# Kernel optimization log

Hardware: AMD Instinct MI355X
Metric: run time of the kernel (lower is better)

The kernel has to match this reference:

```python
import jax, jax.numpy as jnp
import numpy as np

B, S, D, H = 2, 2048, 512, 8


def setup_inputs() -> dict:
    key = jax.random.key(0)
    ks = jax.random.split(key, 9)
    scale = 1.0 / np.sqrt(D)
    x = jax.random.normal(ks[0], (B, S, D), dtype=jnp.float32)
    # Per-head full-width projections, stacked over heads: [H, D, D]
    Wq = jax.random.normal(ks[1], (H, D, D), dtype=jnp.float32) * scale
    Wk = jax.random.normal(ks[2], (H, D, D), dtype=jnp.float32) * scale
    Wv = jax.random.normal(ks[3], (H, D, D), dtype=jnp.float32) * scale
    bq = jax.random.normal(ks[4], (H, D), dtype=jnp.float32) * 0.01
    bk = jax.random.normal(ks[5], (H, D), dtype=jnp.float32) * 0.01
    bv = jax.random.normal(ks[6], (H, D), dtype=jnp.float32) * 0.01
    Wo = jax.random.normal(ks[7], (H * D, D), dtype=jnp.float32) * (1.0 / np.sqrt(H * D))
    bo = jax.random.normal(ks[8], (D,), dtype=jnp.float32) * 0.01
    return {"x": x, "Wq": Wq, "bq": bq, "Wk": Wk, "bk": bk, "Wv": Wv, "bv": bv, "Wo": Wo, "bo": bo}


def reference(x, Wq, bq, Wk, bk, Wv, bv, Wo, bo):
    # Batched per-head projections: [B,S,D] x [H,D,E] -> [B,H,S,E]
    q = jnp.einsum('bsd,hde->bhse', x, Wq) + bq[None, :, None, :]
    k = jnp.einsum('bsd,hde->bhse', x, Wk) + bk[None, :, None, :]
    v = jnp.einsum('bsd,hde->bhse', x, Wv) + bv[None, :, None, :]
    # NOTE: original module has NO 1/sqrt(d) scaling
    scores = jnp.einsum('bhse,bhte->bhst', q, k)  # [B,H,S,S]
    attn = jax.nn.softmax(scores, axis=-1)
    out = jnp.einsum('bhst,bhte->bhse', attn, v)  # [B,H,S,D]
    # Concat heads along feature dim: [B,S,H*D]
    cat = out.transpose(0, 2, 1, 3).reshape(B, S, H * D)
    return cat @ Wo + bo
```

## Files before the change

### kernel.cpp

```cpp
#include <hip/hip_runtime.h>

typedef _Float16 f16;
typedef _Float16 f16x8 __attribute__((ext_vector_type(8)));
typedef float f32x4 __attribute__((ext_vector_type(4)));

#define B_ 2
#define S_ 2048
#define D_ 512
#define H_ 8

__device__ inline void async_ld16(const void* g, void* l) {
  __builtin_amdgcn_global_load_lds((__attribute__((address_space(1))) void*)(g),
                                   (__attribute__((address_space(3))) void*)(l),
                                   16, 0, 0);
}

__global__ __launch_bounds__(256) void cvt_f16(const float* __restrict__ src,
                                               f16* __restrict__ dst, long n) {
  long i = (long)blockIdx.x * 256 + threadIdx.x;
  if (i >= n) return;
  dst[i] = (f16)src[i];
}

__global__ __launch_bounds__(256) void transpose_f32(const float* __restrict__ src,
                                                     f16* __restrict__ dst, int R, int C) {
  __shared__ float t[32][33];
  size_t zoff = (size_t)blockIdx.z * R * C;
  const float* s = src + zoff;
  int tx = threadIdx.x;
  int ty = threadIdx.y;
  int c0 = blockIdx.x * 32, r0 = blockIdx.y * 32;
#pragma unroll
  for (int i = 0; i < 4; ++i)
    t[ty + i * 8][tx] = s[(size_t)(r0 + ty + i * 8) * C + c0 + tx];
  __syncthreads();
#pragma unroll
  for (int i = 0; i < 4; ++i)
    dst[zoff + (size_t)(c0 + ty + i * 8) * R + r0 + tx] = (f16)t[tx][ty + i * 8];
}

__global__ __launch_bounds__(256) void reduce_out(const float* __restrict__ part,
                                                  const float* __restrict__ bo,
                                                  float* __restrict__ out, long n, int nslab) {
  long i = (long)blockIdx.x * 256 + threadIdx.x;
  if (i >= n) return;
  float v = bo[i & (D_ - 1)];
  for (int s = 0; s < nslab; ++s) v += part[(long)s * n + i];
  out[i] = v;
}

struct GemmArgs {
  const f16 *A, *Bm;
  void* C;
  const float* bias;
  float* Mloc;
  int K, lda, ldb, ldc;
  int zbase, NG, PBG;
  long sAp, sAb, sAg, sAz;
  long sBp, sBb, sBg, sBz;
  long sCp, sCb, sCg, sCz;
  long sbp, sbb, sbg, sbz;
  long sMlz;
};

template <typename OutT, int BIAS, bool PEXP>
__global__ __launch_bounds__(256) void gemm_nt(GemmArgs p) {
  int zloc = blockIdx.z;
  int zi = p.zbase + zloc;
  int pp = zi / p.PBG; int rz = zi - pp * p.PBG;
  int bb = rz / p.NG;  int g = rz - bb * p.NG;
  const f16* A  = p.A + (pp * p.sAp + bb * p.sAb + g * p.sAg + (long)zloc * p.sAz);
  const f16* Bm = p.Bm + (pp * p.sBp + bb * p.sBb + g * p.sBg + (long)zloc * p.sBz);
  OutT* C = (OutT*)p.C + (pp * p.sCp + bb * p.sCb + g * p.sCg + (long)zloc * p.sCz);
  const float* bias = nullptr;
  if (BIAS) bias = p.bias + (pp * p.sbp + bb * p.sbb + g * p.sbg + (long)zloc * p.sbz);

  __shared__ f16 lA[4096];
  __shared__ f16 lB[4096];
  __shared__ float lMx[PEXP ? 256 : 1];
  __shared__ f16 lR[PEXP ? 32 * 136 : 1];

  int tid = threadIdx.x;
  int lane = tid & 63;
  int w = tid >> 6;
  int wm = (w >> 1) << 6;
  int wn = (w & 1) << 6;
  long bm = (long)blockIdx.y * 128;
  long bn = (long)blockIdx.x * 128;

  f32x4 acc[4][4] = {};
  int qd = lane >> 4;
  int fr = lane & 15;

  int q0 = tid, q1 = tid + 256;
  int r0s = q0 >> 2, c0s = (q0 & 3) ^ ((r0s >> 1) & 3);
  int r1s = q1 >> 2, c1s = (q1 & 3) ^ ((r1s >> 1) & 3);

  for (int k0 = 0; k0 < p.K; k0 += 32) {
    long oa0 = (bm + r0s) * (long)p.lda + (k0 + c0s * 8);
    long oa1 = (bm + r1s) * (long)p.lda + (k0 + c1s * 8);
    long ob0 = (bn + r0s) * (long)p.ldb + (k0 + c0s * 8);
    long ob1 = (bn + r1s) * (long)p.ldb + (k0 + c1s * 8);
    __syncthreads();
    async_ld16(A + oa0,  lA + (size_t)q0 * 8);
    async_ld16(A + oa1,  lA + (size_t)q1 * 8);
    async_ld16(Bm + ob0, lB + (size_t)q0 * 8);
    async_ld16(Bm + ob1, lB + (size_t)q1 * 8);
    __syncthreads();

    f16x8 ah[4], bh[4];
#pragma unroll
    for (int i = 0; i < 4; ++i) {
      int m = wm + i * 16 + fr;
      ah[i] = *(const f16x8*)(lA + ((size_t)m * 4 + (qd ^ ((m >> 1) & 3))) * 8);
      int n = wn + i * 16 + fr;
      bh[i] = *(const f16x8*)(lB + ((size_t)n * 4 + (qd ^ ((n >> 1) & 3))) * 8);
    }
#pragma unroll
    for (int i = 0; i < 4; ++i)
#pragma unroll
      for (int j = 0; j < 4; ++j)
        acc[i][j] = __builtin_amdgcn_mfma_f32_16x16x32_f16(ah[i], bh[j], acc[i][j], 0, 0, 0);
  }

  int rr0 = qd * 4;
  if (PEXP) {
#pragma unroll
    for (int i = 0; i < 4; ++i) {
#pragma unroll
      for (int r = 0; r < 4; ++r) {
        float v = fmaxf(fmaxf(acc[i][0][r], acc[i][1][r]),
                        fmaxf(acc[i][2][r], acc[i][3][r]));
        v = fmaxf(v, __shfl_xor(v, 1, 64));
        v = fmaxf(v, __shfl_xor(v, 2, 64));
        v = fmaxf(v, __shfl_xor(v, 4, 64));
        v = fmaxf(v, __shfl_xor(v, 8, 64));
        if (fr == 0) lMx[(w & 1) * 128 + wm + i * 16 + rr0 + r] = v;
      }
    }
    __syncthreads();
    if (tid < 128) {
      float ml = fmaxf(lMx[tid], lMx[128 + tid]);
      p.Mloc[(long)zloc * p.sMlz + (long)blockIdx.x * S_ + bm + tid] = ml;
    }
    int rowBase = (w >> 1) << 4;
#pragma unroll
    for (int i = 0; i < 4; ++i) {
      __syncthreads();
#pragma unroll
      for (int r = 0; r < 4; ++r) {
        int rl = wm + i * 16 + rr0 + r;
        float ml = fmaxf(lMx[rl], lMx[128 + rl]);
        int rowLoc = rowBase + rr0 + r;
#pragma unroll
        for (int j = 0; j < 4; ++j) {
          int col = wn + j * 16 + fr;
          lR[rowLoc * 136 + col] = (f16)__expf(acc[i][j][r] - ml);
        }
      }
      __syncthreads();
      int rowLoc = tid >> 3;
      int colLoc = (tid & 7) * 16;
      long grow = bm + ((rowLoc & 15) + i * 16) + ((long)(rowLoc >> 4) << 6);
      f16x8 v0 = *(const f16x8*)(lR + rowLoc * 136 + colLoc);
      f16x8 v1 = *(const f16x8*)(lR + rowLoc * 136 + colLoc + 8);
      f16* dst = (f16*)C + grow * (long)p.ldc + bn + colLoc;
      *(f16x8*)(dst) = v0;
      *(f16x8*)(dst + 8) = v1;
    }
  } else {
#pragma unroll
    for (int i = 0; i < 4; ++i) {
#pragma unroll
      for (int j = 0; j < 4; ++j) {
#pragma unroll
        for (int r = 0; r < 4; ++r) {
          long row = bm + wm + i * 16 + rr0 + r;
          long col = bn + wn + j * 16 + fr;
          float v = acc[i][j][r];
          if (BIAS == 1) v += bias[col];
          if (BIAS == 2) v += bias[row];
          C[row * (long)p.ldc + col] = (OutT)v;
        }
      }
    }
  }
}

struct QkvArgs {
  const f16 *xh, *wqk, *wv;
  f16 *qk, *vT;
  const float *bqk, *bv;
};
__global__ __launch_bounds__(256) void qkv_proj(QkvArgs p) {
  const long SD = (long)S_ * D_, DD = (long)D_ * D_, DS = (long)D_ * S_;
  int zi = blockIdx.z;
  int pp = zi >> 4;
  int r = zi & 15;
  int b = r >> 3, h = r & 7;
  int bid = blockIdx.x;
  const f16 *A, *Bm;
  f16* C;
  const float* bias;
  long bm, bn;
  int ldc;
  bool biasRow;
  if (pp < 2) {
    A = p.xh + (long)b * SD;
    Bm = p.wqk + ((long)pp * 8 + h) * DD;
    C = p.qk + (long)zi * SD;
    bias = p.bqk + ((long)pp * 8 + h) * D_;
    bm = (long)(bid >> 2) * 128; bn = (long)(bid & 3) * 128;
    ldc = D_; biasRow = false;
  } else {
    A = p.wv + (long)h * DD;
    Bm = p.xh + (long)b * SD;
    C = p.vT + (long)(b * 8 + h) * DS;
    bias = p.bv + (long)h * D_;
    bm = (long)(bid >> 4) * 128; bn = (long)(bid & 15) * 128;
    ldc = S_; biasRow = true;
  }

  __shared__ f16 lA[4096];
  __shared__ f16 lB[4096];

  int tid = threadIdx.x;
  int lane = tid & 63;
  int w = tid >> 6;
  int wm = (w >> 1) << 6;
  int wn = (w & 1) << 6;

  f32x4 acc[4][4] = {};
  int qd = lane >> 4;
  int fr = lane & 15;

  int q0 = tid, q1 = tid + 256;
  int r0s = q0 >> 2, c0s = (q0 & 3) ^ ((r0s >> 1) & 3);
  int r1s = q1 >> 2, c1s = (q1 & 3) ^ ((r1s >> 1) & 3);

  for (int k0 = 0; k0 < D_; k0 += 32) {
    long oa0 = (bm + r0s) * (long)D_ + (k0 + c0s * 8);
    long oa1 = (bm + r1s) * (long)D_ + (k0 + c1s * 8);
    long ob0 = (bn + r0s) * (long)D_ + (k0 + c0s * 8);
    long ob1 = (bn + r1s) * (long)D_ + (k0 + c1s * 8);
    __syncthreads();
    async_ld16(A + oa0,  lA + (size_t)q0 * 8);
    async_ld16(A + oa1,  lA + (size_t)q1 * 8);
    async_ld16(Bm + ob0, lB + (size_t)q0 * 8);
    async_ld16(Bm + ob1, lB + (size_t)q1 * 8);
    __syncthreads();

    f16x8 ah[4], bh[4];
#pragma unroll
    for (int i = 0; i < 4; ++i) {
      int m = wm + i * 16 + fr;
      ah[i] = *(const f16x8*)(lA + ((size_t)m * 4 + (qd ^ ((m >> 1) & 3))) * 8);
      int n = wn + i * 16 + fr;
      bh[i] = *(const f16x8*)(lB + ((size_t)n * 4 + (qd ^ ((n >> 1) & 3))) * 8);
    }
#pragma unroll
    for (int i = 0; i < 4; ++i)
#pragma unroll
      for (int j = 0; j < 4; ++j)
        acc[i][j] = __builtin_amdgcn_mfma_f32_16x16x32_f16(ah[i], bh[j], acc[i][j], 0, 0, 0);
  }

  int rr0 = qd * 4;
#pragma unroll
  for (int i = 0; i < 4; ++i) {
#pragma unroll
    for (int j = 0; j < 4; ++j) {
#pragma unroll
      for (int r = 0; r < 4; ++r) {
        long row = bm + wm + i * 16 + rr0 + r;
        long col = bn + wn + j * 16 + fr;
        float v = acc[i][j][r] + (biasRow ? bias[row] : bias[col]);
        C[row * (long)ldc + col] = (f16)v;
      }
    }
  }
}

struct PvArgs {
  const f16* S; const float* Ml; const f16* V; f16* C;
  int ldc, zbase, NG;
  long sVz, sCb, sCg;
};
__global__ __launch_bounds__(256) void pv_flash(PvArgs p) {
  int zloc = blockIdx.z;
  int zi = p.zbase + zloc;
  int bb = zi / p.NG; int g = zi - bb * p.NG;
  const f16* Sm = p.S + (long)zloc * S_ * S_;
  const float* Ml = p.Ml + (long)zloc * 16 * S_;
  const f16* V = p.V + (long)zloc * p.sVz;
  f16* C = p.C + bb * p.sCb + g * p.sCg;

  __shared__ f16 lP[64 * 32];
  __shared__ f16 lV[256 * 32];

  int tid = threadIdx.x;
  int lane = tid & 63;
  int w = tid >> 6;
  long bm = (long)blockIdx.y * 64;
  long bn = (long)blockIdx.x * 256;
  int e0 = w << 6;

  int qd = lane >> 4;
  int fr = lane & 15;

  f32x4 acc[4][4] = {};
  f32x4 lacc[4] = {};
  f16x8 ones;
#pragma unroll
  for (int j = 0; j < 8; ++j) ones[j] = (f16)1.0f;

  float mg[4];
#pragma unroll
  for (int i = 0; i < 4; ++i) {
    float m = -1e30f;
#pragma unroll
    for (int cb = 0; cb < 16; ++cb)
      m = fmaxf(m, Ml[cb * S_ + bm + i * 16 + fr]);
    mg[i] = m;
  }
  f16 al16[4];

  int rs = tid >> 2, cs = (tid & 3) ^ ((rs >> 1) & 3);

  for (int k0 = 0; k0 < S_; k0 += 32) {
    if ((k0 & 127) == 0) {
      int cb = k0 >> 7;
#pragma unroll
      for (int i = 0; i < 4; ++i)
        al16[i] = (f16)__expf(Ml[cb * S_ + bm + i * 16 + fr] - mg[i]);
    }
    __syncthreads();
    async_ld16(Sm + (bm + rs) * (long)S_ + (k0 + cs * 8), lP + (size_t)tid * 8);
#pragma unroll
    for (int j = 0; j < 4; ++j) {
      int q = j * 256 + tid;
      int rv = q >> 2, cv = (q & 3) ^ ((rv >> 1) & 3);
      async_ld16(V + (bn + rv) * (long)S_ + (k0 + cv * 8), lV + (size_t)q * 8);
    }
    __syncthreads();

    f16x8 ah[4], bh[4];
#pragma unroll
    for (int i = 0; i < 4; ++i) {
      int m = i * 16 + fr;
      ah[i] = *(const f16x8*)(lP + ((size_t)m * 4 + (qd ^ ((m >> 1) & 3))) * 8);
#pragma unroll
      for (int j = 0; j < 8; ++j) ah[i][j] *= al16[i];
    }
#pragma unroll
    for (int j = 0; j < 4; ++j) {
      int n = e0 + j * 16 + fr;
      bh[j] = *(const f16x8*)(lV + ((size_t)n * 4 + (qd ^ ((n >> 1) & 3))) * 8);
    }
#pragma unroll
    for (int i = 0; i < 4; ++i) {
      lacc[i] = __builtin_amdgcn_mfma_f32_16x16x32_f16(ah[i], ones, lacc[i], 0, 0, 0);
#pragma unroll
      for (int j = 0; j < 4; ++j)
        acc[i][j] = __builtin_amdgcn_mfma_f32_16x16x32_f16(ah[i], bh[j], acc[i][j], 0, 0, 0);
    }
  }

  int rr0 = (lane >> 4) * 4;
#pragma unroll
  for (int i = 0; i < 4; ++i) {
    float inv[4];
#pragma unroll
    for (int r = 0; r < 4; ++r) inv[r] = 1.0f / lacc[i][r];
#pragma unroll
    for (int j = 0; j < 4; ++j) {
#pragma unroll
      for (int r = 0; r < 4; ++r) {
        long row = bm + i * 16 + rr0 + r;
        long col = bn + e0 + j * 16 + fr;
        C[row * (long)p.ldc + col] = (f16)(acc[i][j][r] * inv[r]);
      }
    }
  }
}

extern "C" void kernel_launch(void* const* d_in, const int* in_sizes, int n_in,
                              void* d_out, int out_size, void* d_ws, size_t ws_size,
                              hipStream_t stream) {
  const float* x  = (const float*)d_in[0];
  const float* Wq = (const float*)d_in[1];
  const float* bq = (const float*)d_in[2];
  const float* Wk = (const float*)d_in[3];
  const float* bk = (const float*)d_in[4];
  const float* Wv = (const float*)d_in[5];
  const float* bv = (const float*)d_in[6];
  const float* Wo = (const float*)d_in[7];
  const float* bo = (const float*)d_in[8];
  float* out = (float*)d_out;

  auto al = [](size_t v) { return (v + 255) & ~(size_t)255; };
  const size_t eX = (size_t)B_ * S_ * D_;
  const size_t eW = (size_t)H_ * D_ * D_;
  const size_t eSS = (size_t)S_ * S_;
  const long SD = (long)S_ * D_;
  const long DD = (long)D_ * D_;
  const long DS = (long)D_ * S_;

  size_t fixed = al(eX * 2) + al(2 * eW * 2) + al(eW * 2) + al(eW * 2)
               + al(2ULL * H_ * D_ * 4);
  int NB = 1, GH = 1, GS = 1; bool found = false;
  for (int nb = 2; nb >= 1 && !found; --nb)
    for (int gh = 8; gh >= 1 && !found; gh >>= 1)
      for (int gs = nb * gh; gs >= 1 && !found; gs >>= 1) {
        size_t need = fixed + al((size_t)nb * S_ * H_ * D_ * 2)
                    + al(2ULL * nb * gh * S_ * D_ * 2)
                    + al((size_t)nb * gh * D_ * S_ * 2)
                    + al(4ULL * nb * SD * 4)
                    + al((size_t)gs * eSS * 2)
                    + al((size_t)gs * 16 * S_ * 4);
        if (need <= ws_size) { NB = nb; GH = gh; GS = gs; found = true; }
      }

  char* p0 = (char*)d_ws;
  size_t off = 0;
  f16* xh    = (f16*)(p0 + off); off += al(eX * 2);
  f16* wqk   = (f16*)(p0 + off); off += al(2 * eW * 2);
  f16* wv    = (f16*)(p0 + off); off += al(eW * 2);
  f16* wo    = (f16*)(p0 + off); off += al(eW * 2);
  float* bqk = (float*)(p0 + off); off += al(2ULL * H_ * D_ * 4);
  f16* catb  = (f16*)(p0 + off); off += al((size_t)NB * S_ * H_ * D_ * 2);
  f16* qk    = (f16*)(p0 + off); off += al(2ULL * NB * GH * S_ * D_ * 2);
  f16* vT    = (f16*)(p0 + off); off += al((size_t)NB * GH * D_ * S_ * 2);
  float* opart = (float*)(p0 + off); off += al(4ULL * NB * SD * 4);
  f16* scores = (f16*)(p0 + off); off += al((size_t)GS * eSS * 2);
  float* mloc = (float*)(p0 + off);

  cvt_f16<<<dim3((unsigned)((eX + 255) / 256)), 256, 0, stream>>>(x, xh, (long)eX);
  dim3 tb(32, 8, 1);
  transpose_f32<<<dim3(16, 16, H_), tb, 0, stream>>>(Wq, wqk, D_, D_);
  transpose_f32<<<dim3(16, 16, H_), tb, 0, stream>>>(Wk, wqk + eW, D_, D_);
  transpose_f32<<<dim3(16, 16, H_), tb, 0, stream>>>(Wv, wv, D_, D_);
  transpose_f32<<<dim3(16, 128, 1), tb, 0, stream>>>(Wo, wo, H_ * D_, D_);
  hipMemcpyAsync(bqk, bq, (size_t)H_ * D_ * 4, hipMemcpyDeviceToDevice, stream);
  hipMemcpyAsync(bqk + H_ * D_, bk, (size_t)H_ * D_ * 4, hipMemcpyDeviceToDevice, stream);

  for (int b0 = 0; b0 < B_; b0 += NB) {
    for (int h0 = 0; h0 < H_; h0 += GH) {
      if (NB == 2 && GH == 8) {
        QkvArgs a{xh, wqk, wv, qk, vT, bqk, bv};
        qkv_proj<<<dim3(64, 1, 48), 256, 0, stream>>>(a);
      } else {
        {
          GemmArgs a{};
          a.A = xh + (long)b0 * SD;
          a.Bm = wqk + (long)h0 * DD;
          a.C = qk; a.bias = bqk + (long)h0 * D_;
          a.K = D_; a.lda = D_; a.ldb = D_; a.ldc = D_;
          a.zbase = 0; a.NG = GH; a.PBG = NB * GH;
          a.sAb = SD;
          a.sBp = (long)H_ * DD; a.sBg = DD;
          a.sCz = SD;
          a.sbp = (long)H_ * D_; a.sbg = D_;
          gemm_nt<f16, 1, false><<<dim3(4, 16, 2 * NB * GH), 256, 0, stream>>>(a);
        }
        {
          GemmArgs a{};
          a.A = wv + (long)h0 * DD; a.Bm = xh + (long)b0 * SD;
          a.C = vT; a.bias = bv + (long)h0 * D_;
          a.K = D_; a.lda = D_; a.ldb = D_; a.ldc = S_;
          a.zbase = 0; a.NG = GH; a.PBG = NB * GH;
          a.sAg = DD;
          a.sBb = SD;
          a.sCz = DS;
          a.sbg = D_;
          gemm_nt<f16, 2, false><<<dim3(16, 4, NB * GH), 256, 0, stream>>>(a);
        }
      }
      for (int g0 = 0; g0 < NB * GH; g0 += GS) {
        {
          GemmArgs a{};
          a.A = qk + (long)g0 * SD;
          a.Bm = qk + ((long)NB * GH + g0) * SD;
          a.C = scores; a.Mloc = mloc;
          a.K = D_; a.lda = D_; a.ldb = D_; a.ldc = S_;
          a.zbase = g0; a.NG = GH; a.PBG = NB * GH;
          a.sAz = SD; a.sBz = SD; a.sCz = (long)eSS;
          a.sMlz = 16L * S_;
          gemm_nt<f16, 0, true><<<dim3(16, 16, GS), 256, 0, stream>>>(a);
        }
        {
          PvArgs a{};
          a.S = scores; a.Ml = mloc; a.V = vT + (long)g0 * DS;
          a.C = catb + (long)h0 * D_;
          a.ldc = H_ * D_; a.zbase = g0; a.NG = GH;
          a.sVz = DS; a.sCb = (long)S_ * H_ * D_; a.sCg = D_;
          pv_flash<<<dim3(2, S_ / 64, GS), 256, 0, stream>>>(a);
        }
      }
    }
    {
      GemmArgs a{};
      a.A = catb; a.Bm = wo;
      a.C = opart;
      a.K = 1024; a.lda = H_ * D_; a.ldb = H_ * D_; a.ldc = D_;
      a.zbase = 0; a.NG = 4; a.PBG = NB * 4;
      a.sAb = (long)S_ * H_ * D_; a.sAg = 1024;
      a.sBg = 1024;
      a.sCb = SD; a.sCg = (long)NB * SD;
      gemm_nt<float, 0, false><<<dim3(4, 16, NB * 4), 256, 0, stream>>>(a);
    }
    reduce_out<<<dim3((unsigned)(((long)NB * SD + 255) / 256)), 256, 0, stream>>>(
        opart, bo, out + (long)b0 * SD, (long)NB * SD, 4);
  }
}
```

Before: 486.7 us.

## Compute softmax row sums in scores epilogue and stage stores through LDS

The scores GEMM epilogue now also reduces per-block exponent row sums and writes them next to the local maxima. The PV kernel rescales and combines these sums instead of running an extra MFMA against a ones vector every K step, which removes a quarter of its matrix work. The QKV projection and PV epilogues now stage results through shared memory so they can be written as 16-byte coalesced rows instead of scattered 2-byte stores. The cost is one more workspace buffer, extra shuffles and barriers, and row sums taken from fp32 exponentials while the PV numerator uses their fp16-rounded values.

```diff
diff --git a/kernel.cpp b/kernel.cpp
--- a/kernel.cpp
+++ b/kernel.cpp
@@ -54,6 +54,7 @@
   void* C;
   const float* bias;
   float* Mloc;
+  float* Lloc;
   int K, lda, ldb, ldc;
   int zbase, NG, PBG;
   long sAp, sAb, sAg, sAz;
@@ -78,6 +79,7 @@
   __shared__ f16 lA[4096];
   __shared__ f16 lB[4096];
   __shared__ float lMx[PEXP ? 256 : 1];
+  __shared__ float lSm[PEXP ? 256 : 1];
   __shared__ f16 lR[PEXP ? 32 * 136 : 1];
 
   int tid = threadIdx.x;
@@ -152,11 +154,19 @@
         int rl = wm + i * 16 + rr0 + r;
         float ml = fmaxf(lMx[rl], lMx[128 + rl]);
         int rowLoc = rowBase + rr0 + r;
+        float rsum = 0.f;
 #pragma unroll
         for (int j = 0; j < 4; ++j) {
           int col = wn + j * 16 + fr;
-          lR[rowLoc * 136 + col] = (f16)__expf(acc[i][j][r] - ml);
+          float e = __expf(acc[i][j][r] - ml);
+          rsum += e;
+          lR[rowLoc * 136 + col] = (f16)e;
         }
+        rsum += __shfl_xor(rsum, 1, 64);
+        rsum += __shfl_xor(rsum, 2, 64);
+        rsum += __shfl_xor(rsum, 4, 64);
+        rsum += __shfl_xor(rsum, 8, 64);
+        if (fr == 0) lSm[(w & 1) * 128 + rl] = rsum;
       }
       __syncthreads();
       int rowLoc = tid >> 3;
@@ -168,6 +178,10 @@
       *(f16x8*)(dst) = v0;
       *(f16x8*)(dst + 8) = v1;
     }
+    __syncthreads();
+    if (tid < 128)
+      p.Lloc[(long)zloc * p.sMlz + (long)blockIdx.x * S_ + bm + tid] =
+          lSm[tid] + lSm[128 + tid];
   } else {
 #pragma unroll
     for (int i = 0; i < 4; ++i) {
@@ -221,8 +235,9 @@
     ldc = S_; biasRow = true;
   }
 
-  __shared__ f16 lA[4096];
-  __shared__ f16 lB[4096];
+  __shared__ f16 lAB[8192];
+  f16* lA = lAB;
+  f16* lB = lAB + 4096;
 
   int tid = threadIdx.x;
   int lane = tid & 63;
@@ -266,23 +281,36 @@
   }
 
   int rr0 = qd * 4;
+  int rowBase = (w >> 1) << 4;
+  f16* lR = lAB;
 #pragma unroll
   for (int i = 0; i < 4; ++i) {
-#pragma unroll
-    for (int j = 0; j < 4; ++j) {
-#pragma unroll
-      for (int r = 0; r < 4; ++r) {
-        long row = bm + wm + i * 16 + rr0 + r;
+    __syncthreads();
+#pragma unroll
+    for (int r = 0; r < 4; ++r) {
+      int rowLoc = rowBase + rr0 + r;
+      long row = bm + wm + i * 16 + rr0 + r;
+#pragma unroll
+      for (int j = 0; j < 4; ++j) {
         long col = bn + wn + j * 16 + fr;
         float v = acc[i][j][r] + (biasRow ? bias[row] : bias[col]);
-        C[row * (long)ldc + col] = (f16)v;
-      }
-    }
+        lR[rowLoc * 136 + wn + j * 16 + fr] = (f16)v;
+      }
+    }
+    __syncthreads();
+    int rowLoc = tid >> 3;
+    int colLoc = (tid & 7) * 16;
+    long grow = bm + ((rowLoc & 15) + i * 16) + ((long)(rowLoc >> 4) << 6);
+    f16x8 v0 = *(const f16x8*)(lR + rowLoc * 136 + colLoc);
+    f16x8 v1 = *(const f16x8*)(lR + rowLoc * 136 + colLoc + 8);
+    f16* dst = C + grow * (long)ldc + bn + colLoc;
+    *(f16x8*)dst = v0;
+    *(f16x8*)(dst + 8) = v1;
   }
 }
 
 struct PvArgs {
-  const f16* S; const float* Ml; const f16* V; f16* C;
+  const f16* S; const float* Ml; const float* Ll; const f16* V; f16* C;
   int ldc, zbase, NG;
   long sVz, sCb, sCg;
 };
@@ -292,6 +320,7 @@
   int bb = zi / p.NG; int g = zi - bb * p.NG;
   const f16* Sm = p.S + (long)zloc * S_ * S_;
   const float* Ml = p.Ml + (long)zloc * 16 * S_;
+  const float* Ll = p.Ll + (long)zloc * 16 * S_;
   const f16* V = p.V + (long)zloc * p.sVz;
   f16* C = p.C + bb * p.sCb + g * p.sCg;
 
@@ -307,21 +336,26 @@
 
   int qd = lane >> 4;
   int fr = lane & 15;
+  int rr0 = qd * 4;
 
   f32x4 acc[4][4] = {};
-  f32x4 lacc[4] = {};
-  f16x8 ones;
-#pragma unroll
-  for (int j = 0; j < 8; ++j) ones[j] = (f16)1.0f;
-
-  float mg[4];
+
+  float mg[4], lsum[4];
 #pragma unroll
   for (int i = 0; i < 4; ++i) {
+    float mv[16];
     float m = -1e30f;
 #pragma unroll
+    for (int cb = 0; cb < 16; ++cb) {
+      mv[cb] = Ml[cb * S_ + bm + i * 16 + fr];
+      m = fmaxf(m, mv[cb]);
+    }
+    mg[i] = m;
+    float s = 0.f;
+#pragma unroll
     for (int cb = 0; cb < 16; ++cb)
-      m = fmaxf(m, Ml[cb * S_ + bm + i * 16 + fr]);
-    mg[i] = m;
+      s += Ll[cb * S_ + bm + i * 16 + fr] * __expf(mv[cb] - m);
+    lsum[i] = s;
   }
   f16 al16[4];
 
@@ -358,29 +392,34 @@
       bh[j] = *(const f16x8*)(lV + ((size_t)n * 4 + (qd ^ ((n >> 1) & 3))) * 8);
     }
 #pragma unroll
-    for (int i = 0; i < 4; ++i) {
-      lacc[i] = __builtin_amdgcn_mfma_f32_16x16x32_f16(ah[i], ones, lacc[i], 0, 0, 0);
+    for (int i = 0; i < 4; ++i)
 #pragma unroll
       for (int j = 0; j < 4; ++j)
         acc[i][j] = __builtin_amdgcn_mfma_f32_16x16x32_f16(ah[i], bh[j], acc[i][j], 0, 0, 0);
-    }
-  }
-
-  int rr0 = (lane >> 4) * 4;
+  }
+
+  f16* lR = lV;
 #pragma unroll
   for (int i = 0; i < 4; ++i) {
+    __syncthreads();
     float inv[4];
 #pragma unroll
-    for (int r = 0; r < 4; ++r) inv[r] = 1.0f / lacc[i][r];
-#pragma unroll
-    for (int j = 0; j < 4; ++j) {
-#pragma unroll
-      for (int r = 0; r < 4; ++r) {
-        long row = bm + i * 16 + rr0 + r;
-        long col = bn + e0 + j * 16 + fr;
-        C[row * (long)p.ldc + col] = (f16)(acc[i][j][r] * inv[r]);
-      }
-    }
+    for (int r = 0; r < 4; ++r)
+      inv[r] = 1.0f / __shfl(lsum[i], (lane & 48) + rr0 + r, 64);
+#pragma unroll
+    for (int j = 0; j < 4; ++j)
+#pragma unroll
+      for (int r = 0; r < 4; ++r)
+        lR[(rr0 + r) * 264 + e0 + j * 16 + fr] = (f16)(acc[i][j][r] * inv[r]);
+    __syncthreads();
+    int rowLoc = tid >> 4;
+    int colLoc = (tid & 15) * 16;
+    long grow = bm + i * 16 + rowLoc;
+    f16x8 v0 = *(const f16x8*)(lR + rowLoc * 264 + colLoc);
+    f16x8 v1 = *(const f16x8*)(lR + rowLoc * 264 + colLoc + 8);
+    f16* dst = C + grow * (long)p.ldc + bn + colLoc;
+    *(f16x8*)dst = v0;
+    *(f16x8*)(dst + 8) = v1;
   }
 }
 
@@ -417,7 +456,7 @@
                     + al((size_t)nb * gh * D_ * S_ * 2)
                     + al(4ULL * nb * SD * 4)
                     + al((size_t)gs * eSS * 2)
-                    + al((size_t)gs * 16 * S_ * 4);
+                    + 2 * al((size_t)gs * 16 * S_ * 4);
         if (need <= ws_size) { NB = nb; GH = gh; GS = gs; found = true; }
       }
 
@@ -433,7 +472,8 @@
   f16* vT    = (f16*)(p0 + off); off += al((size_t)NB * GH * D_ * S_ * 2);
   float* opart = (float*)(p0 + off); off += al(4ULL * NB * SD * 4);
   f16* scores = (f16*)(p0 + off); off += al((size_t)GS * eSS * 2);
-  float* mloc = (float*)(p0 + off);
+  float* mloc = (float*)(p0 + off); off += al((size_t)GS * 16 * S_ * 4);
+  float* lloc = (float*)(p0 + off);
 
   cvt_f16<<<dim3((unsigned)((eX + 255) / 256)), 256, 0, stream>>>(x, xh, (long)eX);
   dim3 tb(32, 8, 1);
@@ -481,7 +521,7 @@
           GemmArgs a{};
           a.A = qk + (long)g0 * SD;
           a.Bm = qk + ((long)NB * GH + g0) * SD;
-          a.C = scores; a.Mloc = mloc;
+          a.C = scores; a.Mloc = mloc; a.Lloc = lloc;
           a.K = D_; a.lda = D_; a.ldb = D_; a.ldc = S_;
           a.zbase = g0; a.NG = GH; a.PBG = NB * GH;
           a.sAz = SD; a.sBz = SD; a.sCz = (long)eSS;
@@ -490,7 +530,7 @@
         }
         {
           PvArgs a{};
-          a.S = scores; a.Ml = mloc; a.V = vT + (long)g0 * DS;
+          a.S = scores; a.Ml = mloc; a.Ll = lloc; a.V = vT + (long)g0 * DS;
           a.C = catb + (long)h0 * D_;
           a.ldc = H_ * D_; a.zbase = g0; a.NG = GH;
           a.sVz = DS; a.sCb = (long)S_ * H_ * D_; a.sCg = D_;
```

Result: slower. 588.8 us (+21.0%).

## Double-buffer LDS tiles in GEMM and PV kernels to overlap loads with MFMA

Applied to the files above, without the earlier changes.

Converts the single-buffered async global-to-LDS K-loops in the generic GEMM, the QKV projection GEMM and the PV flash kernel into a two-stage ping-pong pipeline. The next tile is prefetched right after the barrier while MFMAs run on the current tile, so each iteration needs one barrier instead of two. The PEXP epilogue scratch (lMx and lR) now reuses the tile buffers after an extra barrier rather than having its own allocation. In exchange, LDS per block roughly doubles, which may lower occupancy.

```diff
diff --git a/kernel.cpp b/kernel.cpp
--- a/kernel.cpp
+++ b/kernel.cpp
@@ -75,10 +75,8 @@
   const float* bias = nullptr;
   if (BIAS) bias = p.bias + (pp * p.sbp + bb * p.sbb + g * p.sbg + (long)zloc * p.sbz);
 
-  __shared__ f16 lA[4096];
-  __shared__ f16 lB[4096];
-  __shared__ float lMx[PEXP ? 256 : 1];
-  __shared__ f16 lR[PEXP ? 32 * 136 : 1];
+  __shared__ __attribute__((aligned(16))) f16 lA[2][4096];
+  __shared__ __attribute__((aligned(16))) f16 lB[2][4096];
 
   int tid = threadIdx.x;
   int lane = tid & 63;
@@ -96,35 +94,41 @@
   int r0s = q0 >> 2, c0s = (q0 & 3) ^ ((r0s >> 1) & 3);
   int r1s = q1 >> 2, c1s = (q1 & 3) ^ ((r1s >> 1) & 3);
 
-  for (int k0 = 0; k0 < p.K; k0 += 32) {
-    long oa0 = (bm + r0s) * (long)p.lda + (k0 + c0s * 8);
-    long oa1 = (bm + r1s) * (long)p.lda + (k0 + c1s * 8);
-    long ob0 = (bn + r0s) * (long)p.ldb + (k0 + c0s * 8);
-    long ob1 = (bn + r1s) * (long)p.ldb + (k0 + c1s * 8);
+  auto stage = [&](int buf, int k0) {
+    async_ld16(A + (bm + r0s) * (long)p.lda + (k0 + c0s * 8), lA[buf] + (size_t)q0 * 8);
+    async_ld16(A + (bm + r1s) * (long)p.lda + (k0 + c1s * 8), lA[buf] + (size_t)q1 * 8);
+    async_ld16(Bm + (bn + r0s) * (long)p.ldb + (k0 + c0s * 8), lB[buf] + (size_t)q0 * 8);
+    async_ld16(Bm + (bn + r1s) * (long)p.ldb + (k0 + c1s * 8), lB[buf] + (size_t)q1 * 8);
+  };
+
+  int nt = p.K >> 5;
+  stage(0, 0);
+  int cur = 0;
+  for (int t = 0; t < nt; ++t) {
     __syncthreads();
-    async_ld16(A + oa0,  lA + (size_t)q0 * 8);
-    async_ld16(A + oa1,  lA + (size_t)q1 * 8);
-    async_ld16(Bm + ob0, lB + (size_t)q0 * 8);
-    async_ld16(Bm + ob1, lB + (size_t)q1 * 8);
-    __syncthreads();
+    if (t + 1 < nt) stage(cur ^ 1, (t + 1) << 5);
 
     f16x8 ah[4], bh[4];
 #pragma unroll
     for (int i = 0; i < 4; ++i) {
       int m = wm + i * 16 + fr;
-      ah[i] = *(const f16x8*)(lA + ((size_t)m * 4 + (qd ^ ((m >> 1) & 3))) * 8);
+      ah[i] = *(const f16x8*)(lA[cur] + ((size_t)m * 4 + (qd ^ ((m >> 1) & 3))) * 8);
       int n = wn + i * 16 + fr;
-      bh[i] = *(const f16x8*)(lB + ((size_t)n * 4 + (qd ^ ((n >> 1) & 3))) * 8);
+      bh[i] = *(const f16x8*)(lB[cur] + ((size_t)n * 4 + (qd ^ ((n >> 1) & 3))) * 8);
     }
 #pragma unroll
     for (int i = 0; i < 4; ++i)
 #pragma unroll
       for (int j = 0; j < 4; ++j)
         acc[i][j] = __builtin_amdgcn_mfma_f32_16x16x32_f16(ah[i], bh[j], acc[i][j], 0, 0, 0);
+    cur ^= 1;
   }
 
   int rr0 = qd * 4;
   if (PEXP) {
+    __syncthreads();
+    float* lMx = (float*)lA;
+    f16* lR = (f16*)lB;
 #pragma unroll
     for (int i = 0; i < 4; ++i) {
 #pragma unroll
@@ -221,8 +225,8 @@
     ldc = S_; biasRow = true;
   }
 
-  __shared__ f16 lA[4096];
-  __shared__ f16 lB[4096];
+  __shared__ __attribute__((aligned(16))) f16 lA[2][4096];
+  __shared__ __attribute__((aligned(16))) f16 lB[2][4096];
 
   int tid = threadIdx.x;
   int lane = tid & 63;
@@ -238,31 +242,33 @@
   int r0s = q0 >> 2, c0s = (q0 & 3) ^ ((r0s >> 1) & 3);
   int r1s = q1 >> 2, c1s = (q1 & 3) ^ ((r1s >> 1) & 3);
 
-  for (int k0 = 0; k0 < D_; k0 += 32) {
-    long oa0 = (bm + r0s) * (long)D_ + (k0 + c0s * 8);
-    long oa1 = (bm + r1s) * (long)D_ + (k0 + c1s * 8);
-    long ob0 = (bn + r0s) * (long)D_ + (k0 + c0s * 8);
-    long ob1 = (bn + r1s) * (long)D_ + (k0 + c1s * 8);
+  auto stage = [&](int buf, int k0) {
+    async_ld16(A + (bm + r0s) * (long)D_ + (k0 + c0s * 8), lA[buf] + (size_t)q0 * 8);
+    async_ld16(A + (bm + r1s) * (long)D_ + (k0 + c1s * 8), lA[buf] + (size_t)q1 * 8);
+    async_ld16(Bm + (bn + r0s) * (long)D_ + (k0 + c0s * 8), lB[buf] + (size_t)q0 * 8);
+    async_ld16(Bm + (bn + r1s) * (long)D_ + (k0 + c1s * 8), lB[buf] + (size_t)q1 * 8);
+  };
+
+  stage(0, 0);
+  int cur = 0;
+  for (int t = 0; t < (D_ >> 5); ++t) {
     __syncthreads();
-    async_ld16(A + oa0,  lA + (size_t)q0 * 8);
-    async_ld16(A + oa1,  lA + (size_t)q1 * 8);
-    async_ld16(Bm + ob0, lB + (size_t)q0 * 8);
-    async_ld16(Bm + ob1, lB + (size_t)q1 * 8);
-    __syncthreads();
+    if (t + 1 < (D_ >> 5)) stage(cur ^ 1, (t + 1) << 5);
 
     f16x8 ah[4], bh[4];
 #pragma unroll
     for (int i = 0; i < 4; ++i) {
       int m = wm + i * 16 + fr;
-      ah[i] = *(const f16x8*)(lA + ((size_t)m * 4 + (qd ^ ((m >> 1) & 3))) * 8);
+      ah[i] = *(const f16x8*)(lA[cur] + ((size_t)m * 4 + (qd ^ ((m >> 1) & 3))) * 8);
       int n = wn + i * 16 + fr;
-      bh[i] = *(const f16x8*)(lB + ((size_t)n * 4 + (qd ^ ((n >> 1) & 3))) * 8);
+      bh[i] = *(const f16x8*)(lB[cur] + ((size_t)n * 4 + (qd ^ ((n >> 1) & 3))) * 8);
     }
 #pragma unroll
     for (int i = 0; i < 4; ++i)
 #pragma unroll
       for (int j = 0; j < 4; ++j)
         acc[i][j] = __builtin_amdgcn_mfma_f32_16x16x32_f16(ah[i], bh[j], acc[i][j], 0, 0, 0);
+    cur ^= 1;
   }
 
   int rr0 = qd * 4;
@@ -295,8 +301,8 @@
   const f16* V = p.V + (long)zloc * p.sVz;
   f16* C = p.C + bb * p.sCb + g * p.sCg;
 
-  __shared__ f16 lP[64 * 32];
-  __shared__ f16 lV[256 * 32];
+  __shared__ __attribute__((aligned(16))) f16 lP[2][2048];
+  __shared__ __attribute__((aligned(16))) f16 lV[2][8192];
 
   int tid = threadIdx.x;
   int lane = tid & 63;
@@ -327,6 +333,18 @@
 
   int rs = tid >> 2, cs = (tid & 3) ^ ((rs >> 1) & 3);
 
+  auto stage = [&](int buf, int k0) {
+    async_ld16(Sm + (bm + rs) * (long)S_ + (k0 + cs * 8), lP[buf] + (size_t)tid * 8);
+#pragma unroll
+    for (int j = 0; j < 4; ++j) {
+      int q = j * 256 + tid;
+      int rv = q >> 2, cv = (q & 3) ^ ((rv >> 1) & 3);
+      async_ld16(V + (bn + rv) * (long)S_ + (k0 + cv * 8), lV[buf] + (size_t)q * 8);
+    }
+  };
+
+  stage(0, 0);
+  int cur = 0;
   for (int k0 = 0; k0 < S_; k0 += 32) {
     if ((k0 & 127) == 0) {
       int cb = k0 >> 7;
@@ -335,27 +353,20 @@
         al16[i] = (f16)__expf(Ml[cb * S_ + bm + i * 16 + fr] - mg[i]);
     }
     __syncthreads();
-    async_ld16(Sm + (bm + rs) * (long)S_ + (k0 + cs * 8), lP + (size_t)tid * 8);
-#pragma unroll
-    for (int j = 0; j < 4; ++j) {
-      int q = j * 256 + tid;
-      int rv = q >> 2, cv = (q & 3) ^ ((rv >> 1) & 3);
-      async_ld16(V + (bn + rv) * (long)S_ + (k0 + cv * 8), lV + (size_t)q * 8);
-    }
-    __syncthreads();
+    if (k0 + 32 < S_) stage(cur ^ 1, k0 + 32);
 
     f16x8 ah[4], bh[4];
 #pragma unroll
     for (int i = 0; i < 4; ++i) {
       int m = i * 16 + fr;
-      ah[i] = *(const f16x8*)(lP + ((size_t)m * 4 + (qd ^ ((m >> 1) & 3))) * 8);
+      ah[i] = *(const f16x8*)(lP[cur] + ((size_t)m * 4 + (qd ^ ((m >> 1) & 3))) * 8);
 #pragma unroll
       for (int j = 0; j < 8; ++j) ah[i][j] *= al16[i];
     }
 #pragma unroll
     for (int j = 0; j < 4; ++j) {
       int n = e0 + j * 16 + fr;
-      bh[j] = *(const f16x8*)(lV + ((size_t)n * 4 + (qd ^ ((n >> 1) & 3))) * 8);
+      bh[j] = *(const f16x8*)(lV[cur] + ((size_t)n * 4 + (qd ^ ((n >> 1) & 3))) * 8);
     }
 #pragma unroll
     for (int i = 0; i < 4; ++i) {
@@ -364,6 +375,7 @@
       for (int j = 0; j < 4; ++j)
         acc[i][j] = __builtin_amdgcn_mfma_f32_16x16x32_f16(ah[i], bh[j], acc[i][j], 0, 0, 0);
     }
+    cur ^= 1;
   }
 
   int rr0 = (lane >> 4) * 4;
```

Result: slower. 501.4 us (+3.0%).
